# Kernel tuning notes

Measured on AMD Instinct MI355X. Metric: run time of the kernel, lower is better.

The kernel has to match this reference:

```python
import jax, jax.numpy as jnp
import numpy as np

N = 100000
E = 1600000
F_IN = 128
HID = 128
CLS = 40


def setup_inputs() -> dict:
    key = jax.random.key(0)
    ks = jax.random.split(key, 8)
    x = jax.random.normal(ks[0], (N, F_IN), dtype=jnp.float32)
    edge_index = jax.random.randint(ks[1], (2, E), 0, N, dtype=jnp.int64)
    s1 = 1.0 / np.sqrt(F_IN)
    s2 = 1.0 / np.sqrt(HID)
    return {
        "x": x,
        "edge_index": edge_index,
        "Wl1": jax.random.uniform(ks[2], (F_IN, HID), jnp.float32, -s1, s1),
        "Wr1": jax.random.uniform(ks[3], (F_IN, HID), jnp.float32, -s1, s1),
        "b1": jnp.zeros((HID,), jnp.float32),
        "Wl2": jax.random.uniform(ks[4], (HID, CLS), jnp.float32, -s2, s2),
        "Wr2": jax.random.uniform(ks[5], (HID, CLS), jnp.float32, -s2, s2),
        "b2": jnp.zeros((CLS,), jnp.float32),
    }


def _sage_conv(x, src, dst, Wl, Wr, b):
    # mean aggregation of neighbor features: messages flow src -> dst
    msg = x[src]                                                  # [E, F]
    agg = jax.ops.segment_sum(msg, dst, num_segments=N)          # [N, F]
    deg = jax.ops.segment_sum(jnp.ones((src.shape[0],), x.dtype), dst,
                              num_segments=N)                     # [N]
    mean = agg / jnp.maximum(deg, 1.0)[:, None]
    # PyG SAGEConv: lin_l(aggregated) + lin_r(root); bias on lin_l only
    return mean @ Wl + x @ Wr + b


def reference(x, edge_index, Wl1, Wr1, b1, Wl2, Wr2, b2):
    src, dst = edge_index[0], edge_index[1]
    h = _sage_conv(x, src, dst, Wl1, Wr1, b1)
    h = jax.nn.relu(h)
    # dropout is identity in eval mode
    out = _sage_conv(h, src, dst, Wl2, Wr2, b2)
    return out
```

## Files before the change

### kernel.cpp

```cpp
#include <hip/hip_runtime.h>

#define F 128
#define CLSN 40
#define NFINE_MAX 256
#define PCAP 10240
#define TILE 4096
#define STAGE_CAP 10240
#define QSCALE 22.0f

typedef __attribute__((ext_vector_type(8))) short short8v;
typedef __attribute__((ext_vector_type(4))) float float4v;

static __device__ inline ushort f2bf(float f) {
  uint u = __float_as_uint(f);
  uint r = (u + 0x7FFFu + ((u >> 16) & 1u)) >> 16;
  return (ushort)r;
}
static __device__ inline float bfLo(uint u) { return __uint_as_float(u << 16); }
static __device__ inline float bfHi(uint u) { return __uint_as_float(u & 0xFFFF0000u); }
static __device__ inline int sb(uint v, int sh) { return (int)(signed char)(v >> sh); }
static __device__ inline unsigned char q8(float f) {
  float t = rintf(f * QSCALE);
  t = fminf(fmaxf(t, -127.f), 127.f);
  return (unsigned char)(signed char)(int)t;
}

__global__ __launch_bounds__(256) void k_cast(const float* __restrict__ in,
                                              ushort* __restrict__ outb,
                                              unsigned char* __restrict__ outq, int nelem4) {
  int i = blockIdx.x * 256 + threadIdx.x;
  if (i < nelem4) {
    float4 v = reinterpret_cast<const float4*>(in)[i];
    ushort4 o;
    o.x = f2bf(v.x); o.y = f2bf(v.y); o.z = f2bf(v.z); o.w = f2bf(v.w);
    reinterpret_cast<ushort4*>(outb)[i] = o;
    uchar4 q;
    q.x = q8(v.x); q.y = q8(v.y); q.z = q8(v.z); q.w = q8(v.w);
    reinterpret_cast<uchar4*>(outq)[i] = q;
  }
}

__global__ __launch_bounds__(256) void k_pack_w1(const float* __restrict__ Wl,
                                                 const float* __restrict__ Wr,
                                                 ushort* __restrict__ Wp) {
  int t = blockIdx.x * 256 + threadIdx.x;
  if (t >= 4096) return;
  int lane = t & 63, f = (t >> 6) & 7, ks = t >> 9;
  int col = f * 16 + (lane & 15);
  int k0 = ks * 32 + (lane >> 4) * 8;
#pragma unroll
  for (int j = 0; j < 8; ++j) {
    int k = k0 + j;
    float w = (k < 128) ? Wl[k * 128 + col] : Wr[(k - 128) * 128 + col];
    Wp[t * 8 + j] = f2bf(w);
  }
}

__global__ __launch_bounds__(256) void k_pack_w2pair(const float* __restrict__ Wl,
                                                     const float* __restrict__ Wr,
                                                     ushort* __restrict__ Wpl,
                                                     ushort* __restrict__ Wpr) {
  int t = blockIdx.x * 256 + threadIdx.x;
  if (t >= 1536) return;
  const float* W = (t < 768) ? Wl : Wr;
  ushort* Wp = (t < 768) ? Wpl : Wpr;
  int tt = (t < 768) ? t : t - 768;
  int lane = tt & 63, rem = tt >> 6;
  int f = rem % 3, ks = rem / 3;
  int col = f * 16 + (lane & 15);
  int k0 = ks * 32 + (lane >> 4) * 8;
#pragma unroll
  for (int j = 0; j < 8; ++j) {
    int k = k0 + j;
    float w = (col < CLSN) ? W[k * CLSN + col] : 0.f;
    Wp[tt * 8 + j] = f2bf(w);
  }
}

__global__ void k_init_fcur(int* __restrict__ fcur, int nfine) {
  int i = blockIdx.x * 256 + threadIdx.x;
  if (i < nfine) fcur[i] = i * PCAP;
}

__global__ __launch_bounds__(256) void k_partition(const int* __restrict__ src,
                                                   const int* __restrict__ dst,
                                                   int* __restrict__ fcur,
                                                   uint* __restrict__ pairs, int E) {
  __shared__ int hh[NFINE_MAX];
  __shared__ int bb[NFINE_MAX];
  __shared__ unsigned char ebkt[TILE];
  __shared__ ushort dlow[TILE];
  const int tid = threadIdx.x;
  const int tile0 = blockIdx.x * TILE;
  const int lim = min(TILE, E - tile0);
  for (int i = tid; i < NFINE_MAX; i += 256) hh[i] = 0;
  __syncthreads();
  for (int i = tid; i < lim; i += 256) {
    int d = dst[tile0 + i];
    int b = d >> 9;
    ebkt[i] = (unsigned char)b;
    dlow[i] = (ushort)(d & 511);
    atomicAdd(&hh[b], 1);
  }
  __syncthreads();
  for (int i = tid; i < NFINE_MAX; i += 256) {
    int c = hh[i];
    bb[i] = c ? atomicAdd(&fcur[i], c) : 0;
    hh[i] = 0;
  }
  __syncthreads();
  for (int i = tid; i < lim; i += 256) {
    int b = ebkt[i];
    int r = atomicAdd(&hh[b], 1);
    uint p = (uint)src[tile0 + i] | ((uint)dlow[i] << 17);
    pairs[bb[b] + r] = p;
  }
}

__global__ __launch_bounds__(256) void k_scan_fine(const int* __restrict__ fcur,
                                                   int* __restrict__ fbase,
                                                   int nfine, int E) {
  __shared__ int s[256];
  int tid = threadIdx.x;
  int v = (tid < nfine) ? (fcur[tid] - tid * PCAP) : 0;
  s[tid] = v;
  __syncthreads();
  for (int d = 1; d < 256; d <<= 1) {
    int u = (tid >= d) ? s[tid - d] : 0;
    __syncthreads();
    s[tid] += u;
    __syncthreads();
  }
  if (tid < nfine) fbase[tid] = s[tid] - v;
  if (tid == 0) fbase[nfine] = E;
}

__global__ __launch_bounds__(256) void k_local_scatter(const uint* __restrict__ pairs,
                                                       const int* __restrict__ fcur,
                                                       const int* __restrict__ fbase,
                                                       int* __restrict__ offsets,
                                                       int* __restrict__ srcs,
                                                       int n, int E) {
  __shared__ int s_cnt[512];
  __shared__ int s_scan[512];
  __shared__ int s_stage[STAGE_CAP];
  const int b = blockIdx.x, tid = threadIdx.x;
  const int node0 = b << 9;
  const int pbase = b * PCAP;
  const int ebase = fbase[b];
  const int ecnt = fcur[b] - pbase;
  s_cnt[tid] = 0;
  s_cnt[tid + 256] = 0;
  __syncthreads();
  for (int i = tid; i < ecnt; i += 256) atomicAdd(&s_cnt[pairs[pbase + i] >> 17], 1);
  __syncthreads();
  s_scan[tid] = s_cnt[tid];
  s_scan[tid + 256] = s_cnt[tid + 256];
  __syncthreads();
  for (int d = 1; d < 512; d <<= 1) {
    int v0 = (tid >= d) ? s_scan[tid - d] : 0;
    int v1 = (tid + 256 >= d) ? s_scan[tid + 256 - d] : 0;
    __syncthreads();
    s_scan[tid] += v0;
    s_scan[tid + 256] += v1;
    __syncthreads();
  }
  int e0 = s_scan[tid] - s_cnt[tid];
  int e1 = s_scan[tid + 256] - s_cnt[tid + 256];
  if (node0 + tid < n) offsets[node0 + tid] = ebase + e0;
  if (node0 + tid + 256 < n) offsets[node0 + tid + 256] = ebase + e1;
  if (b == gridDim.x - 1 && tid == 0) offsets[n] = E;
  __syncthreads();
  s_cnt[tid] = e0;
  s_cnt[tid + 256] = e1;
  __syncthreads();
  for (int i = tid; i < ecnt; i += 256) {
    uint p = pairs[pbase + i];
    int v = (int)(p >> 17);
    int s = (int)(p & 0x1FFFFu);
    int pos = atomicAdd(&s_cnt[v], 1);
    if (pos < STAGE_CAP) s_stage[pos] = s;
    else srcs[ebase + pos] = s;
  }
  __syncthreads();
  int lim = min(ecnt, STAGE_CAP);
  for (int i = tid; i < lim; i += 256) srcs[ebase + i] = s_stage[i];
}

__global__ __launch_bounds__(256) void k_agg_x(const unsigned char* __restrict__ xq,
                                               const int* __restrict__ offsets,
                                               const int* __restrict__ srcs,
                                               ushort* __restrict__ mean, int n) {
  const int wid = (blockIdx.x * 256 + threadIdx.x) >> 6;
  const int lane = threadIdx.x & 63;
  const int g = lane >> 4, cl = lane & 15;
  const int node = wid * 4 + g;
  if (node >= n) return;
  const uint2* fp = reinterpret_cast<const uint2*>(xq);
  const int beg = offsets[node];
  const int deg = offsets[node + 1] - beg;
  int s0 = 0, s1 = 0, s2 = 0, s3 = 0, s4 = 0, s5 = 0, s6 = 0, s7 = 0;
  for (int chunk = 0; chunk < deg; chunk += 16) {
    int cnt = min(16, deg - chunk);
    int s = (cl < cnt) ? srcs[beg + chunk + cl] : 0;
    int k = 0;
    for (; k + 7 < cnt; k += 8) {
      int r0 = __shfl(s, g * 16 + k);
      int r1 = __shfl(s, g * 16 + k + 1);
      int r2 = __shfl(s, g * 16 + k + 2);
      int r3 = __shfl(s, g * 16 + k + 3);
      int r4 = __shfl(s, g * 16 + k + 4);
      int r5 = __shfl(s, g * 16 + k + 5);
      int r6 = __shfl(s, g * 16 + k + 6);
      int r7 = __shfl(s, g * 16 + k + 7);
      uint2 v0 = fp[(size_t)r0 * 16 + cl];
      uint2 v1 = fp[(size_t)r1 * 16 + cl];
      uint2 v2 = fp[(size_t)r2 * 16 + cl];
      uint2 v3 = fp[(size_t)r3 * 16 + cl];
      uint2 v4 = fp[(size_t)r4 * 16 + cl];
      uint2 v5 = fp[(size_t)r5 * 16 + cl];
      uint2 v6 = fp[(size_t)r6 * 16 + cl];
      uint2 v7 = fp[(size_t)r7 * 16 + cl];
      s0 += sb(v0.x, 0) + sb(v1.x, 0) + sb(v2.x, 0) + sb(v3.x, 0) +
            sb(v4.x, 0) + sb(v5.x, 0) + sb(v6.x, 0) + sb(v7.x, 0);
      s1 += sb(v0.x, 8) + sb(v1.x, 8) + sb(v2.x, 8) + sb(v3.x, 8) +
            sb(v4.x, 8) + sb(v5.x, 8) + sb(v6.x, 8) + sb(v7.x, 8);
      s2 += sb(v0.x, 16) + sb(v1.x, 16) + sb(v2.x, 16) + sb(v3.x, 16) +
            sb(v4.x, 16) + sb(v5.x, 16) + sb(v6.x, 16) + sb(v7.x, 16);
      s3 += sb(v0.x, 24) + sb(v1.x, 24) + sb(v2.x, 24) + sb(v3.x, 24) +
            sb(v4.x, 24) + sb(v5.x, 24) + sb(v6.x, 24) + sb(v7.x, 24);
      s4 += sb(v0.y, 0) + sb(v1.y, 0) + sb(v2.y, 0) + sb(v3.y, 0) +
            sb(v4.y, 0) + sb(v5.y, 0) + sb(v6.y, 0) + sb(v7.y, 0);
      s5 += sb(v0.y, 8) + sb(v1.y, 8) + sb(v2.y, 8) + sb(v3.y, 8) +
            sb(v4.y, 8) + sb(v5.y, 8) + sb(v6.y, 8) + sb(v7.y, 8);
      s6 += sb(v0.y, 16) + sb(v1.y, 16) + sb(v2.y, 16) + sb(v3.y, 16) +
            sb(v4.y, 16) + sb(v5.y, 16) + sb(v6.y, 16) + sb(v7.y, 16);
      s7 += sb(v0.y, 24) + sb(v1.y, 24) + sb(v2.y, 24) + sb(v3.y, 24) +
            sb(v4.y, 24) + sb(v5.y, 24) + sb(v6.y, 24) + sb(v7.y, 24);
    }
    for (; k < cnt; ++k) {
      int r0 = __shfl(s, g * 16 + k);
      uint2 v0 = fp[(size_t)r0 * 16 + cl];
      s0 += sb(v0.x, 0); s1 += sb(v0.x, 8);
      s2 += sb(v0.x, 16); s3 += sb(v0.x, 24);
      s4 += sb(v0.y, 0); s5 += sb(v0.y, 8);
      s6 += sb(v0.y, 16); s7 += sb(v0.y, 24);
    }
  }
  float inv = deg > 0 ? 1.f / (QSCALE * (float)deg) : 0.f;
  uint4 o;
  o.x = (uint)f2bf((float)s0 * inv) | ((uint)f2bf((float)s1 * inv) << 16);
  o.y = (uint)f2bf((float)s2 * inv) | ((uint)f2bf((float)s3 * inv) << 16);
  o.z = (uint)f2bf((float)s4 * inv) | ((uint)f2bf((float)s5 * inv) << 16);
  o.w = (uint)f2bf((float)s6 * inv) | ((uint)f2bf((float)s7 * inv) << 16);
  reinterpret_cast<uint4*>(mean)[(size_t)node * 16 + cl] = o;
}

__global__ __launch_bounds__(256) void k_agg_p(const ushort* __restrict__ p,
                                               const int* __restrict__ offsets,
                                               const int* __restrict__ srcs,
                                               float* __restrict__ m, int n) {
  const int wid = (blockIdx.x * 256 + threadIdx.x) >> 6;
  const int lane = threadIdx.x & 63;
  const int g = lane >> 3, cl = lane & 7;
  const int node = wid * 8 + g;
  if (node >= n) return;
  const uint4* pp = reinterpret_cast<const uint4*>(p);
  const int beg = offsets[node];
  const int deg = offsets[node + 1] - beg;
  float a0 = 0.f, a1 = 0.f, a2 = 0.f, a3 = 0.f;
  float a4 = 0.f, a5 = 0.f, a6 = 0.f, a7 = 0.f;
  for (int chunk = 0; chunk < deg; chunk += 8) {
    int cnt = min(8, deg - chunk);
    int s = (cl < cnt) ? srcs[beg + chunk + cl] : 0;
    int k = 0;
    for (; k + 7 < cnt; k += 8) {
      int r0 = __shfl(s, g * 8 + k);
      int r1 = __shfl(s, g * 8 + k + 1);
      int r2 = __shfl(s, g * 8 + k + 2);
      int r3 = __shfl(s, g * 8 + k + 3);
      int r4 = __shfl(s, g * 8 + k + 4);
      int r5 = __shfl(s, g * 8 + k + 5);
      int r6 = __shfl(s, g * 8 + k + 6);
      int r7 = __shfl(s, g * 8 + k + 7);
      uint4 v0 = pp[(size_t)r0 * 8 + cl];
      uint4 v1 = pp[(size_t)r1 * 8 + cl];
      uint4 v2 = pp[(size_t)r2 * 8 + cl];
      uint4 v3 = pp[(size_t)r3 * 8 + cl];
      uint4 v4 = pp[(size_t)r4 * 8 + cl];
      uint4 v5 = pp[(size_t)r5 * 8 + cl];
      uint4 v6 = pp[(size_t)r6 * 8 + cl];
      uint4 v7 = pp[(size_t)r7 * 8 + cl];
      a0 += bfLo(v0.x) + bfLo(v1.x) + bfLo(v2.x) + bfLo(v3.x) +
            bfLo(v4.x) + bfLo(v5.x) + bfLo(v6.x) + bfLo(v7.x);
      a1 += bfHi(v0.x) + bfHi(v1.x) + bfHi(v2.x) + bfHi(v3.x) +
            bfHi(v4.x) + bfHi(v5.x) + bfHi(v6.x) + bfHi(v7.x);
      a2 += bfLo(v0.y) + bfLo(v1.y) + bfLo(v2.y) + bfLo(v3.y) +
            bfLo(v4.y) + bfLo(v5.y) + bfLo(v6.y) + bfLo(v7.y);
      a3 += bfHi(v0.y) + bfHi(v1.y) + bfHi(v2.y) + bfHi(v3.y) +
            bfHi(v4.y) + bfHi(v5.y) + bfHi(v6.y) + bfHi(v7.y);
      a4 += bfLo(v0.z) + bfLo(v1.z) + bfLo(v2.z) + bfLo(v3.z) +
            bfLo(v4.z) + bfLo(v5.z) + bfLo(v6.z) + bfLo(v7.z);
      a5 += bfHi(v0.z) + bfHi(v1.z) + bfHi(v2.z) + bfHi(v3.z) +
            bfHi(v4.z) + bfHi(v5.z) + bfHi(v6.z) + bfHi(v7.z);
      a6 += bfLo(v0.w) + bfLo(v1.w) + bfLo(v2.w) + bfLo(v3.w) +
            bfLo(v4.w) + bfLo(v5.w) + bfLo(v6.w) + bfLo(v7.w);
      a7 += bfHi(v0.w) + bfHi(v1.w) + bfHi(v2.w) + bfHi(v3.w) +
            bfHi(v4.w) + bfHi(v5.w) + bfHi(v6.w) + bfHi(v7.w);
    }
    for (; k < cnt; ++k) {
      int r0 = __shfl(s, g * 8 + k);
      uint4 v0 = pp[(size_t)r0 * 8 + cl];
      a0 += bfLo(v0.x); a1 += bfHi(v0.x);
      a2 += bfLo(v0.y); a3 += bfHi(v0.y);
      a4 += bfLo(v0.z); a5 += bfHi(v0.z);
      a6 += bfLo(v0.w); a7 += bfHi(v0.w);
    }
  }
  float inv = deg > 0 ? 1.f / (float)deg : 0.f;
  float4* mp = reinterpret_cast<float4*>(m);
  mp[(size_t)node * 16 + cl * 2] = make_float4(a0 * inv, a1 * inv, a2 * inv, a3 * inv);
  mp[(size_t)node * 16 + cl * 2 + 1] = make_float4(a4 * inv, a5 * inv, a6 * inv, a7 * inv);
}

__global__ __launch_bounds__(256) void k_mfma1(const ushort* __restrict__ meanb,
                                               const ushort* __restrict__ rootb,
                                               const ushort* __restrict__ Wp,
                                               const float* __restrict__ b,
                                               ushort* __restrict__ h, int nrows) {
  __shared__ __align__(16) ushort As[64 * 256];
  const int tid = threadIdx.x;
  const int row0 = blockIdx.x * 64;
#pragma unroll
  for (int i = 0; i < 8; ++i) {
    int c = tid + i * 256;
    int r = c >> 5;
    int c16 = c & 31;
    int grow = row0 + r;
    short8v v = {0, 0, 0, 0, 0, 0, 0, 0};
    if (grow < nrows) {
      const ushort* srcp = (c16 < 16) ? (meanb + (size_t)grow * 128 + c16 * 8)
                                      : (rootb + (size_t)grow * 128 + (c16 - 16) * 8);
      v = *reinterpret_cast<const short8v*>(srcp);
    }
    int dbyte = r * 512 + ((c16 * 16) ^ ((r & 7) << 4));
    *reinterpret_cast<short8v*>(reinterpret_cast<char*>(As) + dbyte) = v;
  }
  __syncthreads();
  const int lane = tid & 63;
  const int rbase = (tid >> 6) * 16;
  const int arow = rbase + (lane & 15);
  const int axor = (arow & 7) << 4;
  const short8v* Wp8 = reinterpret_cast<const short8v*>(Wp);
  float4v acc[8];
#pragma unroll
  for (int f = 0; f < 8; ++f) acc[f] = {0.f, 0.f, 0.f, 0.f};
#pragma unroll
  for (int ks = 0; ks < 8; ++ks) {
    int abyte = arow * 512 + ((ks * 64 + (lane >> 4) * 16) ^ axor);
    short8v a = *reinterpret_cast<const short8v*>(reinterpret_cast<const char*>(As) + abyte);
#pragma unroll
    for (int f = 0; f < 8; ++f) {
      short8v bf = Wp8[(ks * 8 + f) * 64 + lane];
      acc[f] = __builtin_amdgcn_mfma_f32_16x16x32_bf16(a, bf, acc[f], 0, 0, 0);
    }
  }
  const int col_lo = lane & 15;
  const int rq = (lane >> 4) * 4;
#pragma unroll
  for (int f = 0; f < 8; ++f) {
    int col = f * 16 + col_lo;
    float bias = b[col];
#pragma unroll
    for (int r = 0; r < 4; ++r) {
      int row = row0 + rbase + rq + r;
      if (row < nrows) {
        float vv = fmaxf(acc[f][r] + bias, 0.f);
        h[(size_t)row * 128 + col] = f2bf(vv);
      }
    }
  }
}

__global__ __launch_bounds__(256) void k_proj2(const ushort* __restrict__ hb,
                                               const ushort* __restrict__ Wp,
                                               ushort* __restrict__ p, int nrows) {
  __shared__ __align__(16) ushort As[64 * 128];
  const int tid = threadIdx.x;
  const int row0 = blockIdx.x * 64;
#pragma unroll
  for (int i = 0; i < 4; ++i) {
    int c = tid + i * 256;
    int r = c >> 4;
    int c16 = c & 15;
    int grow = row0 + r;
    short8v v = {0, 0, 0, 0, 0, 0, 0, 0};
    if (grow < nrows) v = *reinterpret_cast<const short8v*>(hb + (size_t)grow * 128 + c16 * 8);
    int dbyte = r * 256 + ((c16 * 16) ^ ((r & 7) << 4));
    *reinterpret_cast<short8v*>(reinterpret_cast<char*>(As) + dbyte) = v;
  }
  __syncthreads();
  const int lane = tid & 63;
  const int rbase = (tid >> 6) * 16;
  const int arow = rbase + (lane & 15);
  const int axor = (arow & 7) << 4;
  const short8v* Wp8 = reinterpret_cast<const short8v*>(Wp);
  float4v acc[3];
#pragma unroll
  for (int f = 0; f < 3; ++f) acc[f] = {0.f, 0.f, 0.f, 0.f};
#pragma unroll
  for (int ks = 0; ks < 4; ++ks) {
    int abyte = arow * 256 + ((ks * 64 + (lane >> 4) * 16) ^ axor);
    short8v a = *reinterpret_cast<const short8v*>(reinterpret_cast<const char*>(As) + abyte);
#pragma unroll
    for (int f = 0; f < 3; ++f) {
      short8v bf = Wp8[(ks * 3 + f) * 64 + lane];
      acc[f] = __builtin_amdgcn_mfma_f32_16x16x32_bf16(a, bf, acc[f], 0, 0, 0);
    }
  }
  const int col_lo = lane & 15;
  const int rq = (lane >> 4) * 4;
#pragma unroll
  for (int f = 0; f < 3; ++f) {
    int col = f * 16 + col_lo;
#pragma unroll
    for (int r = 0; r < 4; ++r) {
      int row = row0 + rbase + rq + r;
      if (row < nrows) p[(size_t)row * 64 + col] = f2bf(acc[f][r]);
    }
  }
#pragma unroll
  for (int r = 0; r < 4; ++r) {
    int row = row0 + rbase + rq + r;
    if (row < nrows) p[(size_t)row * 64 + 48 + col_lo] = 0;
  }
}

__global__ __launch_bounds__(256) void k_root2(const ushort* __restrict__ hb,
                                               const ushort* __restrict__ Wp,
                                               const float* __restrict__ b,
                                               const float* __restrict__ m,
                                               float* __restrict__ out, int nrows) {
  __shared__ __align__(16) ushort As[64 * 128];
  const int tid = threadIdx.x;
  const int row0 = blockIdx.x * 64;
#pragma unroll
  for (int i = 0; i < 4; ++i) {
    int c = tid + i * 256;
    int r = c >> 4;
    int c16 = c & 15;
    int grow = row0 + r;
    short8v v = {0, 0, 0, 0, 0, 0, 0, 0};
    if (grow < nrows) v = *reinterpret_cast<const short8v*>(hb + (size_t)grow * 128 + c16 * 8);
    int dbyte = r * 256 + ((c16 * 16) ^ ((r & 7) << 4));
    *reinterpret_cast<short8v*>(reinterpret_cast<char*>(As) + dbyte) = v;
  }
  __syncthreads();
  const int lane = tid & 63;
  const int rbase = (tid >> 6) * 16;
  const int arow = rbase + (lane & 15);
  const int axor = (arow & 7) << 4;
  const short8v* Wp8 = reinterpret_cast<const short8v*>(Wp);
  float4v acc[3];
#pragma unroll
  for (int f = 0; f < 3; ++f) acc[f] = {0.f, 0.f, 0.f, 0.f};
#pragma unroll
  for (int ks = 0; ks < 4; ++ks) {
    int abyte = arow * 256 + ((ks * 64 + (lane >> 4) * 16) ^ axor);
    short8v a = *reinterpret_cast<const short8v*>(reinterpret_cast<const char*>(As) + abyte);
#pragma unroll
    for (int f = 0; f < 3; ++f) {
      short8v bf = Wp8[(ks * 3 + f) * 64 + lane];
      acc[f] = __builtin_amdgcn_mfma_f32_16x16x32_bf16(a, bf, acc[f], 0, 0, 0);
    }
  }
  const int col_lo = lane & 15;
  const int rq = (lane >> 4) * 4;
#pragma unroll
  for (int f = 0; f < 3; ++f) {
    int col = f * 16 + col_lo;
    if (col < CLSN) {
      float bias = b[col];
#pragma unroll
      for (int r = 0; r < 4; ++r) {
        int row = row0 + rbase + rq + r;
        if (row < nrows)
          out[(size_t)row * CLSN + col] = acc[f][r] + bias + m[(size_t)row * 64 + col];
      }
    }
  }
}

extern "C" void kernel_launch(void* const* d_in, const int* in_sizes, int n_in,
                              void* d_out, int out_size, void* d_ws, size_t ws_size,
                              hipStream_t stream) {
  const float* x = (const float*)d_in[0];
  const int* ei = (const int*)d_in[1];
  const float* Wl1 = (const float*)d_in[2];
  const float* Wr1 = (const float*)d_in[3];
  const float* b1 = (const float*)d_in[4];
  const float* Wl2 = (const float*)d_in[5];
  const float* Wr2 = (const float*)d_in[6];
  const float* b2 = (const float*)d_in[7];
  float* out = (float*)d_out;

  const int n = in_sizes[0] / F;
  const int E = in_sizes[1] / 2;
  const int* src = ei;
  const int* dst = ei + E;

  const int nfine = (n + 511) >> 9;

  size_t off = 0;
  auto alloc = [&](size_t bytes) {
    size_t cur = off;
    off = (off + bytes + 255) & ~(size_t)255;
    return cur;
  };
  char* w = (char*)d_ws;
  int* offsets = (int*)(w + alloc((size_t)(n + 1) * 4));
  int* srcs = (int*)(w + alloc((size_t)E * 4));
  int* fcur = (int*)(w + alloc(NFINE_MAX * 4));
  int* fbase = (int*)(w + alloc((NFINE_MAX + 1) * 4));
  ushort* xb = (ushort*)(w + alloc((size_t)n * F * 2));
  ushort* hb = (ushort*)(w + alloc((size_t)n * F * 2));
  ushort* meanb = (ushort*)(w + alloc((size_t)n * F * 2));
  ushort* Wp1 = (ushort*)(w + alloc(32768 * 2));
  ushort* Wp2l = (ushort*)(w + alloc(6144 * 2));
  ushort* Wp2r = (ushort*)(w + alloc(6144 * 2));
  (void)ws_size;
  uint* pairs = (uint*)meanb;
  ushort* p64 = meanb;
  float* m64 = (float*)xb;
  unsigned char* xq8 = (unsigned char*)hb;

  k_cast<<<(n * 32 + 255) / 256, 256, 0, stream>>>(x, xb, xq8, n * 32);
  k_pack_w1<<<16, 256, 0, stream>>>(Wl1, Wr1, Wp1);
  k_pack_w2pair<<<6, 256, 0, stream>>>(Wl2, Wr2, Wp2l, Wp2r);

  k_init_fcur<<<1, 256, 0, stream>>>(fcur, nfine);
  k_partition<<<(E + TILE - 1) / TILE, 256, 0, stream>>>(src, dst, fcur, pairs, E);
  k_scan_fine<<<1, 256, 0, stream>>>(fcur, fbase, nfine, E);
  k_local_scatter<<<nfine, 256, 0, stream>>>(pairs, fcur, fbase, offsets, srcs, n, E);

  k_agg_x<<<(n + 15) / 16, 256, 0, stream>>>(xq8, offsets, srcs, meanb, n);
  k_mfma1<<<(n + 63) / 64, 256, 0, stream>>>(meanb, xb, Wp1, b1, hb, n);

  k_proj2<<<(n + 63) / 64, 256, 0, stream>>>(hb, Wp2l, p64, n);
  k_agg_p<<<(n + 31) / 32, 256, 0, stream>>>(p64, offsets, srcs, m64, n);
  k_root2<<<(n + 63) / 64, 256, 0, stream>>>(hb, Wp2r, b2, m64, out, n);
}
```

Before: 201.4 us.

## Quantize layer-2 projections to int8 with dynamic scale and fuse setup kernels

Layer-2 projected features are now quantized to int8 using a global max-abs scale, which k_proj2 computes with an atomicMax. The gather in k_agg_p then reads 8 bytes per lane instead of 16, halving gather bandwidth, at the cost of an extra quantization pass and lower precision. Separately, the cast, weight-pack and fcur-init kernels are merged into one launch, and the fine-bucket scan is folded into k_local_scatter, which reduces the number of kernel launches. Every scatter block now recomputes the scan redundantly.

```diff
diff --git a/kernel.cpp b/kernel.cpp
--- a/kernel.cpp
+++ b/kernel.cpp
@@ -24,62 +24,68 @@
   t = fminf(fmaxf(t, -127.f), 127.f);
   return (unsigned char)(signed char)(int)t;
 }
-
-__global__ __launch_bounds__(256) void k_cast(const float* __restrict__ in,
-                                              ushort* __restrict__ outb,
-                                              unsigned char* __restrict__ outq, int nelem4) {
-  int i = blockIdx.x * 256 + threadIdx.x;
-  if (i < nelem4) {
-    float4 v = reinterpret_cast<const float4*>(in)[i];
-    ushort4 o;
-    o.x = f2bf(v.x); o.y = f2bf(v.y); o.z = f2bf(v.z); o.w = f2bf(v.w);
-    reinterpret_cast<ushort4*>(outb)[i] = o;
-    uchar4 q;
-    q.x = q8(v.x); q.y = q8(v.y); q.z = q8(v.z); q.w = q8(v.w);
-    reinterpret_cast<uchar4*>(outq)[i] = q;
-  }
-}
-
-__global__ __launch_bounds__(256) void k_pack_w1(const float* __restrict__ Wl,
-                                                 const float* __restrict__ Wr,
-                                                 ushort* __restrict__ Wp) {
-  int t = blockIdx.x * 256 + threadIdx.x;
-  if (t >= 4096) return;
-  int lane = t & 63, f = (t >> 6) & 7, ks = t >> 9;
-  int col = f * 16 + (lane & 15);
-  int k0 = ks * 32 + (lane >> 4) * 8;
-#pragma unroll
-  for (int j = 0; j < 8; ++j) {
-    int k = k0 + j;
-    float w = (k < 128) ? Wl[k * 128 + col] : Wr[(k - 128) * 128 + col];
-    Wp[t * 8 + j] = f2bf(w);
-  }
-}
-
-__global__ __launch_bounds__(256) void k_pack_w2pair(const float* __restrict__ Wl,
-                                                     const float* __restrict__ Wr,
-                                                     ushort* __restrict__ Wpl,
-                                                     ushort* __restrict__ Wpr) {
-  int t = blockIdx.x * 256 + threadIdx.x;
-  if (t >= 1536) return;
-  const float* W = (t < 768) ? Wl : Wr;
-  ushort* Wp = (t < 768) ? Wpl : Wpr;
-  int tt = (t < 768) ? t : t - 768;
-  int lane = tt & 63, rem = tt >> 6;
-  int f = rem % 3, ks = rem / 3;
-  int col = f * 16 + (lane & 15);
-  int k0 = ks * 32 + (lane >> 4) * 8;
-#pragma unroll
-  for (int j = 0; j < 8; ++j) {
-    int k = k0 + j;
-    float w = (col < CLSN) ? W[k * CLSN + col] : 0.f;
-    Wp[tt * 8 + j] = f2bf(w);
-  }
-}
-
-__global__ void k_init_fcur(int* __restrict__ fcur, int nfine) {
-  int i = blockIdx.x * 256 + threadIdx.x;
-  if (i < nfine) fcur[i] = i * PCAP;
+static __device__ inline unsigned char q8s(float f, float qs) {
+  float t = rintf(f * qs);
+  t = fminf(fmaxf(t, -127.f), 127.f);
+  return (unsigned char)(signed char)(int)t;
+}
+
+__global__ __launch_bounds__(256) void k_prep(const float* __restrict__ x,
+                                              ushort* __restrict__ xb,
+                                              unsigned char* __restrict__ xq,
+                                              const float* __restrict__ Wl1,
+                                              const float* __restrict__ Wr1,
+                                              ushort* __restrict__ Wp1,
+                                              const float* __restrict__ Wl2,
+                                              const float* __restrict__ Wr2,
+                                              ushort* __restrict__ Wpl,
+                                              ushort* __restrict__ Wpr,
+                                              int* __restrict__ fcur,
+                                              int* __restrict__ scl,
+                                              int nelem4, int castBlocks, int nfine) {
+  const int blk = blockIdx.x;
+  if (blk < castBlocks) {
+    int i = blk * 256 + threadIdx.x;
+    if (i < nelem4) {
+      float4 v = reinterpret_cast<const float4*>(x)[i];
+      ushort4 o;
+      o.x = f2bf(v.x); o.y = f2bf(v.y); o.z = f2bf(v.z); o.w = f2bf(v.w);
+      reinterpret_cast<ushort4*>(xb)[i] = o;
+      uchar4 q;
+      q.x = q8(v.x); q.y = q8(v.y); q.z = q8(v.z); q.w = q8(v.w);
+      reinterpret_cast<uchar4*>(xq)[i] = q;
+    }
+  } else if (blk < castBlocks + 16) {
+    int t = (blk - castBlocks) * 256 + threadIdx.x;
+    int lane = t & 63, f = (t >> 6) & 7, ks = t >> 9;
+    int col = f * 16 + (lane & 15);
+    int k0 = ks * 32 + (lane >> 4) * 8;
+#pragma unroll
+    for (int j = 0; j < 8; ++j) {
+      int k = k0 + j;
+      float w = (k < 128) ? Wl1[k * 128 + col] : Wr1[(k - 128) * 128 + col];
+      Wp1[t * 8 + j] = f2bf(w);
+    }
+  } else if (blk < castBlocks + 22) {
+    int t = (blk - castBlocks - 16) * 256 + threadIdx.x;
+    const float* W = (t < 768) ? Wl2 : Wr2;
+    ushort* Wp = (t < 768) ? Wpl : Wpr;
+    int tt = (t < 768) ? t : t - 768;
+    int lane = tt & 63, rem = tt >> 6;
+    int f = rem % 3, ks = rem / 3;
+    int col = f * 16 + (lane & 15);
+    int k0 = ks * 32 + (lane >> 4) * 8;
+#pragma unroll
+    for (int j = 0; j < 8; ++j) {
+      int k = k0 + j;
+      float w = (col < CLSN) ? W[k * CLSN + col] : 0.f;
+      Wp[tt * 8 + j] = f2bf(w);
+    }
+  } else {
+    int i = threadIdx.x;
+    if (i < nfine) fcur[i] = i * PCAP;
+    if (i == 0) *scl = 0;
+  }
 }
 
 __global__ __launch_bounds__(256) void k_partition(const int* __restrict__ src,
@@ -117,38 +123,29 @@
   }
 }
 
-__global__ __launch_bounds__(256) void k_scan_fine(const int* __restrict__ fcur,
-                                                   int* __restrict__ fbase,
-                                                   int nfine, int E) {
-  __shared__ int s[256];
-  int tid = threadIdx.x;
-  int v = (tid < nfine) ? (fcur[tid] - tid * PCAP) : 0;
-  s[tid] = v;
-  __syncthreads();
-  for (int d = 1; d < 256; d <<= 1) {
-    int u = (tid >= d) ? s[tid - d] : 0;
-    __syncthreads();
-    s[tid] += u;
-    __syncthreads();
-  }
-  if (tid < nfine) fbase[tid] = s[tid] - v;
-  if (tid == 0) fbase[nfine] = E;
-}
-
 __global__ __launch_bounds__(256) void k_local_scatter(const uint* __restrict__ pairs,
                                                        const int* __restrict__ fcur,
-                                                       const int* __restrict__ fbase,
                                                        int* __restrict__ offsets,
                                                        int* __restrict__ srcs,
-                                                       int n, int E) {
+                                                       int n, int E, int nfine) {
   __shared__ int s_cnt[512];
   __shared__ int s_scan[512];
   __shared__ int s_stage[STAGE_CAP];
   const int b = blockIdx.x, tid = threadIdx.x;
   const int node0 = b << 9;
   const int pbase = b * PCAP;
-  const int ebase = fbase[b];
+  int c_i = (tid < nfine) ? (fcur[tid] - tid * PCAP) : 0;
+  s_scan[tid] = c_i;
+  __syncthreads();
+  for (int d = 1; d < 256; d <<= 1) {
+    int u = (tid >= d) ? s_scan[tid - d] : 0;
+    __syncthreads();
+    s_scan[tid] += u;
+    __syncthreads();
+  }
   const int ecnt = fcur[b] - pbase;
+  const int ebase = s_scan[b] - ecnt;
+  __syncthreads();
   s_cnt[tid] = 0;
   s_cnt[tid + 256] = 0;
   __syncthreads();
@@ -256,20 +253,36 @@
   reinterpret_cast<uint4*>(mean)[(size_t)node * 16 + cl] = o;
 }
 
-__global__ __launch_bounds__(256) void k_agg_p(const ushort* __restrict__ p,
+__global__ __launch_bounds__(256) void k_quant_p(const ushort* __restrict__ p,
+                                                 const int* __restrict__ scl,
+                                                 unsigned char* __restrict__ pq, int nelem4) {
+  int i = blockIdx.x * 256 + threadIdx.x;
+  if (i >= nelem4) return;
+  float ma = __int_as_float(*scl);
+  float qs = ma > 0.f ? 127.f / ma : 0.f;
+  uint2 v = reinterpret_cast<const uint2*>(p)[i];
+  uchar4 q;
+  q.x = q8s(bfLo(v.x), qs);
+  q.y = q8s(bfHi(v.x), qs);
+  q.z = q8s(bfLo(v.y), qs);
+  q.w = q8s(bfHi(v.y), qs);
+  reinterpret_cast<uchar4*>(pq)[i] = q;
+}
+
+__global__ __launch_bounds__(256) void k_agg_p(const unsigned char* __restrict__ pq,
                                                const int* __restrict__ offsets,
                                                const int* __restrict__ srcs,
+                                               const int* __restrict__ scl,
                                                float* __restrict__ m, int n) {
   const int wid = (blockIdx.x * 256 + threadIdx.x) >> 6;
   const int lane = threadIdx.x & 63;
   const int g = lane >> 3, cl = lane & 7;
   const int node = wid * 8 + g;
   if (node >= n) return;
-  const uint4* pp = reinterpret_cast<const uint4*>(p);
+  const uint2* pp = reinterpret_cast<const uint2*>(pq);
   const int beg = offsets[node];
   const int deg = offsets[node + 1] - beg;
-  float a0 = 0.f, a1 = 0.f, a2 = 0.f, a3 = 0.f;
-  float a4 = 0.f, a5 = 0.f, a6 = 0.f, a7 = 0.f;
+  int s0 = 0, s1 = 0, s2 = 0, s3 = 0, s4 = 0, s5 = 0, s6 = 0, s7 = 0;
   for (int chunk = 0; chunk < deg; chunk += 8) {
     int cnt = min(8, deg - chunk);
     int s = (cl < cnt) ? srcs[beg + chunk + cl] : 0;
@@ -283,44 +296,47 @@
       int r5 = __shfl(s, g * 8 + k + 5);
       int r6 = __shfl(s, g * 8 + k + 6);
       int r7 = __shfl(s, g * 8 + k + 7);
-      uint4 v0 = pp[(size_t)r0 * 8 + cl];
-      uint4 v1 = pp[(size_t)r1 * 8 + cl];
-      uint4 v2 = pp[(size_t)r2 * 8 + cl];
-      uint4 v3 = pp[(size_t)r3 * 8 + cl];
-      uint4 v4 = pp[(size_t)r4 * 8 + cl];
-      uint4 v5 = pp[(size_t)r5 * 8 + cl];
-      uint4 v6 = pp[(size_t)r6 * 8 + cl];
-      uint4 v7 = pp[(size_t)r7 * 8 + cl];
-      a0 += bfLo(v0.x) + bfLo(v1.x) + bfLo(v2.x) + bfLo(v3.x) +
-            bfLo(v4.x) + bfLo(v5.x) + bfLo(v6.x) + bfLo(v7.x);
-      a1 += bfHi(v0.x) + bfHi(v1.x) + bfHi(v2.x) + bfHi(v3.x) +
-            bfHi(v4.x) + bfHi(v5.x) + bfHi(v6.x) + bfHi(v7.x);
-      a2 += bfLo(v0.y) + bfLo(v1.y) + bfLo(v2.y) + bfLo(v3.y) +
-            bfLo(v4.y) + bfLo(v5.y) + bfLo(v6.y) + bfLo(v7.y);
-      a3 += bfHi(v0.y) + bfHi(v1.y) + bfHi(v2.y) + bfHi(v3.y) +
-            bfHi(v4.y) + bfHi(v5.y) + bfHi(v6.y) + bfHi(v7.y);
-      a4 += bfLo(v0.z) + bfLo(v1.z) + bfLo(v2.z) + bfLo(v3.z) +
-            bfLo(v4.z) + bfLo(v5.z) + bfLo(v6.z) + bfLo(v7.z);
-      a5 += bfHi(v0.z) + bfHi(v1.z) + bfHi(v2.z) + bfHi(v3.z) +
-            bfHi(v4.z) + bfHi(v5.z) + bfHi(v6.z) + bfHi(v7.z);
-      a6 += bfLo(v0.w) + bfLo(v1.w) + bfLo(v2.w) + bfLo(v3.w) +
-            bfLo(v4.w) + bfLo(v5.w) + bfLo(v6.w) + bfLo(v7.w);
-      a7 += bfHi(v0.w) + bfHi(v1.w) + bfHi(v2.w) + bfHi(v3.w) +
-            bfHi(v4.w) + bfHi(v5.w) + bfHi(v6.w) + bfHi(v7.w);
+      uint2 v0 = pp[(size_t)r0 * 8 + cl];
+      uint2 v1 = pp[(size_t)r1 * 8 + cl];
+      uint2 v2 = pp[(size_t)r2 * 8 + cl];
+      uint2 v3 = pp[(size_t)r3 * 8 + cl];
+      uint2 v4 = pp[(size_t)r4 * 8 + cl];
+      uint2 v5 = pp[(size_t)r5 * 8 + cl];
+      uint2 v6 = pp[(size_t)r6 * 8 + cl];
+      uint2 v7 = pp[(size_t)r7 * 8 + cl];
+      s0 += sb(v0.x, 0) + sb(v1.x, 0) + sb(v2.x, 0) + sb(v3.x, 0) +
+            sb(v4.x, 0) + sb(v5.x, 0) + sb(v6.x, 0) + sb(v7.x, 0);
+      s1 += sb(v0.x, 8) + sb(v1.x, 8) + sb(v2.x, 8) + sb(v3.x, 8) +
+            sb(v4.x, 8) + sb(v5.x, 8) + sb(v6.x, 8) + sb(v7.x, 8);
+      s2 += sb(v0.x, 16) + sb(v1.x, 16) + sb(v2.x, 16) + sb(v3.x, 16) +
+            sb(v4.x, 16) + sb(v5.x, 16) + sb(v6.x, 16) + sb(v7.x, 16);
+      s3 += sb(v0.x, 24) + sb(v1.x, 24) + sb(v2.x, 24) + sb(v3.x, 24) +
+            sb(v4.x, 24) + sb(v5.x, 24) + sb(v6.x, 24) + sb(v7.x, 24);
+      s4 += sb(v0.y, 0) + sb(v1.y, 0) + sb(v2.y, 0) + sb(v3.y, 0) +
+            sb(v4.y, 0) + sb(v5.y, 0) + sb(v6.y, 0) + sb(v7.y, 0);
+      s5 += sb(v0.y, 8) + sb(v1.y, 8) + sb(v2.y, 8) + sb(v3.y, 8) +
+            sb(v4.y, 8) + sb(v5.y, 8) + sb(v6.y, 8) + sb(v7.y, 8);
+      s6 += sb(v0.y, 16) + sb(v1.y, 16) + sb(v2.y, 16) + sb(v3.y, 16) +
+            sb(v4.y, 16) + sb(v5.y, 16) + sb(v6.y, 16) + sb(v7.y, 16);
+      s7 += sb(v0.y, 24) + sb(v1.y, 24) + sb(v2.y, 24) + sb(v3.y, 24) +
+            sb(v4.y, 24) + sb(v5.y, 24) + sb(v6.y, 24) + sb(v7.y, 24);
     }
     for (; k < cnt; ++k) {
       int r0 = __shfl(s, g * 8 + k);
-      uint4 v0 = pp[(size_t)r0 * 8 + cl];
-      a0 += bfLo(v0.x); a1 += bfHi(v0.x);
-      a2 += bfLo(v0.y); a3 += bfHi(v0.y);
-      a4 += bfLo(v0.z); a5 += bfHi(v0.z);
-      a6 += bfLo(v0.w); a7 += bfHi(v0.w);
-    }
-  }
-  float inv = deg > 0 ? 1.f / (float)deg : 0.f;
+      uint2 v0 = pp[(size_t)r0 * 8 + cl];
+      s0 += sb(v0.x, 0); s1 += sb(v0.x, 8);
+      s2 += sb(v0.x, 16); s3 += sb(v0.x, 24);
+      s4 += sb(v0.y, 0); s5 += sb(v0.y, 8);
+      s6 += sb(v0.y, 16); s7 += sb(v0.y, 24);
+    }
+  }
+  float ma = __int_as_float(*scl);
+  float inv = deg > 0 ? ma / (127.f * (float)deg) : 0.f;
   float4* mp = reinterpret_cast<float4*>(m);
-  mp[(size_t)node * 16 + cl * 2] = make_float4(a0 * inv, a1 * inv, a2 * inv, a3 * inv);
-  mp[(size_t)node * 16 + cl * 2 + 1] = make_float4(a4 * inv, a5 * inv, a6 * inv, a7 * inv);
+  mp[(size_t)node * 16 + cl * 2] =
+      make_float4((float)s0 * inv, (float)s1 * inv, (float)s2 * inv, (float)s3 * inv);
+  mp[(size_t)node * 16 + cl * 2 + 1] =
+      make_float4((float)s4 * inv, (float)s5 * inv, (float)s6 * inv, (float)s7 * inv);
 }
 
 __global__ __launch_bounds__(256) void k_mfma1(const ushort* __restrict__ meanb,
@@ -384,7 +400,8 @@
 
 __global__ __launch_bounds__(256) void k_proj2(const ushort* __restrict__ hb,
                                                const ushort* __restrict__ Wp,
-                                               ushort* __restrict__ p, int nrows) {
+                                               ushort* __restrict__ p,
+                                               int* __restrict__ scl, int nrows) {
   __shared__ __align__(16) ushort As[64 * 128];
   const int tid = threadIdx.x;
   const int row0 = blockIdx.x * 64;
@@ -420,13 +437,17 @@
   }
   const int col_lo = lane & 15;
   const int rq = (lane >> 4) * 4;
+  float mx = 0.f;
 #pragma unroll
   for (int f = 0; f < 3; ++f) {
     int col = f * 16 + col_lo;
 #pragma unroll
     for (int r = 0; r < 4; ++r) {
       int row = row0 + rbase + rq + r;
-      if (row < nrows) p[(size_t)row * 64 + col] = f2bf(acc[f][r]);
+      if (row < nrows) {
+        p[(size_t)row * 64 + col] = f2bf(acc[f][r]);
+        mx = fmaxf(mx, fabsf(acc[f][r]));
+      }
     }
   }
 #pragma unroll
@@ -434,6 +455,9 @@
     int row = row0 + rbase + rq + r;
     if (row < nrows) p[(size_t)row * 64 + 48 + col_lo] = 0;
   }
+#pragma unroll
+  for (int d = 32; d; d >>= 1) mx = fmaxf(mx, __shfl_xor(mx, d));
+  if (lane == 0) atomicMax(scl, __float_as_int(mx));
 }
 
 __global__ __launch_bounds__(256) void k_root2(const ushort* __restrict__ hb,
@@ -521,7 +545,7 @@
   int* offsets = (int*)(w + alloc((size_t)(n + 1) * 4));
   int* srcs = (int*)(w + alloc((size_t)E * 4));
   int* fcur = (int*)(w + alloc(NFINE_MAX * 4));
-  int* fbase = (int*)(w + alloc((NFINE_MAX + 1) * 4));
+  int* scl = (int*)(w + alloc(256));
   ushort* xb = (ushort*)(w + alloc((size_t)n * F * 2));
   ushort* hb = (ushort*)(w + alloc((size_t)n * F * 2));
   ushort* meanb = (ushort*)(w + alloc((size_t)n * F * 2));
@@ -531,22 +555,24 @@
   (void)ws_size;
   uint* pairs = (uint*)meanb;
   ushort* p64 = meanb;
+  unsigned char* pq8 = (unsigned char*)(meanb + (size_t)n * 64);
   float* m64 = (float*)xb;
   unsigned char* xq8 = (unsigned char*)hb;
 
-  k_cast<<<(n * 32 + 255) / 256, 256, 0, stream>>>(x, xb, xq8, n * 32);
-  k_pack_w1<<<16, 256, 0, stream>>>(Wl1, Wr1, Wp1);
-  k_pack_w2pair<<<6, 256, 0, stream>>>(Wl2, Wr2, Wp2l, Wp2r);
-
-  k_init_fcur<<<1, 256, 0, stream>>>(fcur, nfine);
+  const int castBlocks = (n * 32 + 255) / 256;
+
+  k_prep<<<castBlocks + 23, 256, 0, stream>>>(x, xb, xq8, Wl1, Wr1, Wp1, Wl2, Wr2,
+                                              Wp2l, Wp2r, fcur, scl, n * 32, castBlocks,
+                                              nfine);
+
   k_partition<<<(E + TILE - 1) / TILE, 256, 0, stream>>>(src, dst, fcur, pairs, E);
-  k_scan_fine<<<1, 256, 0, stream>>>(fcur, fbase, nfine, E);
-  k_local_scatter<<<nfine, 256, 0, stream>>>(pairs, fcur, fbase, offsets, srcs, n, E);
+  k_local_scatter<<<nfine, 256, 0, stream>>>(pairs, fcur, offsets, srcs, n, E, nfine);
 
   k_agg_x<<<(n + 15) / 16, 256, 0, stream>>>(xq8, offsets, srcs, meanb, n);
   k_mfma1<<<(n + 63) / 64, 256, 0, stream>>>(meanb, xb, Wp1, b1, hb, n);
 
-  k_proj2<<<(n + 63) / 64, 256, 0, stream>>>(hb, Wp2l, p64, n);
-  k_agg_p<<<(n + 31) / 32, 256, 0, stream>>>(p64, offsets, srcs, m64, n);
+  k_proj2<<<(n + 63) / 64, 256, 0, stream>>>(hb, Wp2l, p64, scl, n);
+  k_quant_p<<<(n * 16 + 255) / 256, 256, 0, stream>>>(p64, scl, pq8, n * 16);
+  k_agg_p<<<(n + 31) / 32, 256, 0, stream>>>(pq8, offsets, srcs, scl, m64, n);
   k_root2<<<(n + 63) / 64, 256, 0, stream>>>(hb, Wp2r, b2, m64, out, n);
 }
```

Measured after the change: 262.2 us. +30.2%, slower.
